# Performance work log

Measured on AMD Instinct MI355X. Metric: run time of the kernel, lower is better.

The kernel has to match this reference:

```python
import jax, jax.numpy as jnp
import numpy as np

HEAD = 16

def setup_inputs() -> dict:
    key = jax.random.key(0)
    k1, k2, k3 = jax.random.split(key, 3)
    B, S, D = 2, 2048, 1024
    x = jax.random.normal(k1, (B, S, D), dtype=jnp.float32)
    w_qkv = jax.random.normal(k2, (D, 3 * D), dtype=jnp.float32) * (1.0 / np.sqrt(D))
    b_qkv = jnp.zeros((3 * D,), dtype=jnp.float32)
    w_out = jax.random.normal(k3, (D, D), dtype=jnp.float32) * (1.0 / np.sqrt(D))
    b_out = jnp.zeros((D,), dtype=jnp.float32)
    return {"x": x, "w_qkv": w_qkv, "b_qkv": b_qkv, "w_out": w_out, "b_out": b_out}


def reference(x, w_qkv, b_qkv, w_out, b_out):
    B, S, D = x.shape
    hd = D // HEAD  # head dim
    qkv = x @ w_qkv + b_qkv                      # [B,S,3D]
    qkv = qkv.reshape(B, S, 3, HEAD, hd)
    qkv = jnp.transpose(qkv, (2, 0, 3, 1, 4))    # [3,B,H,S,hd]
    q, k, v = qkv[0], qkv[1], qkv[2]
    scores = jnp.einsum('bhqd,bhkd->bhqk', q, k)  # [B,H,S,S]
    causal = jnp.triu(jnp.ones((S, S), dtype=bool), k=1)
    scores = jnp.where(causal, -jnp.inf, scores)
    scores = scores / jnp.sqrt(jnp.asarray(hd, dtype=x.dtype))
    attn = jax.nn.softmax(scores, axis=-1)
    z = jnp.einsum('bhqk,bhkd->bhqd', attn, v)   # [B,H,S,hd]
    z = jnp.transpose(z, (0, 2, 1, 3)).reshape(B, S, D)
    out = z @ w_out + b_out
    return out
```

## Files before the change

kernel.cpp:

```cpp
#include <hip/hip_runtime.h>

#define S_LEN  2048
#define NH     16
#define HD     64
#define DMODEL 1024

using bf16x8 = __attribute__((ext_vector_type(8))) __bf16;
using f32x4  = __attribute__((ext_vector_type(4))) float;

__device__ __forceinline__ unsigned short f2bf(float f) {
    unsigned u = __float_as_uint(f);
    u += 0x7FFFu + ((u >> 16) & 1u);
    return (unsigned short)(u >> 16);
}
__device__ __forceinline__ unsigned pk_trunc(float lo, float hi) {
    return __builtin_amdgcn_perm(__float_as_uint(hi), __float_as_uint(lo), 0x07060302u);
}

#define EXP2(x) __builtin_amdgcn_exp2f(x)

#define GLDS16(gsrc, ldst) \
    __builtin_amdgcn_global_load_lds((__attribute__((address_space(1))) void*)(gsrc), \
                                     (__attribute__((address_space(3))) void*)(ldst), 16, 0, 0)

#define WAIT_LGKM0() __builtin_amdgcn_s_waitcnt(0xC07F)

#define ASM_VMCNT(n)  asm volatile("s_waitcnt vmcnt(" #n ")" ::: "memory")
#define ASM_BARRIER() asm volatile("s_barrier" ::: "memory")

__global__ __launch_bounds__(256) void prep_kernel(
    const float* __restrict__ x, const float* __restrict__ w_qkv,
    const float* __restrict__ w_out,
    unsigned short* __restrict__ xb, unsigned short* __restrict__ wqkvT,
    unsigned short* __restrict__ woutT) {
    __shared__ float T[32][33];
    int bx = blockIdx.x;
    if (bx < 4096) {
        int idx = (bx * 256 + threadIdx.x) * 4;
        float4 v = *(const float4*)(x + idx);
        ushort4 o;
        o.x = f2bf(v.x); o.y = f2bf(v.y); o.z = f2bf(v.z); o.w = f2bf(v.w);
        *(ushort4*)(xb + idx) = o;
        return;
    }
    int tb = bx - 4096;
    int tcol = tb & 127, krow = tb >> 7;
    const float* in;
    unsigned short* out;
    int N, nbx;
    if (tcol < 96) { in = w_qkv; out = wqkvT; N = 3072; nbx = tcol; }
    else           { in = w_out; out = woutT; N = 1024; nbx = tcol - 96; }
    int r  = threadIdx.x >> 3;
    int c4 = (threadIdx.x & 7) * 4;
    int kbase = krow * 32, nbase = nbx * 32;
    float4 v = *(const float4*)(in + (size_t)(kbase + r) * N + nbase + c4);
    T[r][c4 + 0] = v.x; T[r][c4 + 1] = v.y; T[r][c4 + 2] = v.z; T[r][c4 + 3] = v.w;
    __syncthreads();
    ushort4 o;
    o.x = f2bf(T[c4 + 0][r]); o.y = f2bf(T[c4 + 1][r]);
    o.z = f2bf(T[c4 + 2][r]); o.w = f2bf(T[c4 + 3][r]);
    *(ushort4*)(out + (size_t)(nbase + r) * 1024 + kbase + c4) = o;
}

template <int NI>
__device__ __forceinline__ void mfma_mainloop64(const unsigned short* __restrict__ A,
                                                const unsigned short* __restrict__ B,
                                                int K, int m0, int n0,
                                                unsigned short* As, unsigned short* Bs,
                                                f32x4 acc[4][NI]) {
    const int lane = threadIdx.x & 63, wave = threadIdx.x >> 6;
    const int quad = lane >> 4, l15 = lane & 15;
    const int wm0 = (wave >> 1) * 64, wn0 = (wave & 1) * (NI * 16);
    const int nt = K >> 6;

    auto stage = [&](int k0, int b) {
        unsigned short* Ad = As + b * 8192;
        unsigned short* Bd = Bs + b * (NI * 2048);
        #pragma unroll
        for (int j = 0; j < 4 + NI; ++j) {
            if (j < 4) {
                int c0 = j * 256 + wave * 64;
                int c  = c0 + lane;
                int r = c >> 3, pc = c & 7, q = pc ^ (r & 7);
                GLDS16(A + (size_t)(m0 + r) * K + k0 + q * 8, Ad + c0 * 8);
            } else {
                int c0 = (j - 4) * 256 + wave * 64;
                int c  = c0 + lane;
                int r = c >> 3, pc = c & 7, q = pc ^ (r & 7);
                GLDS16(B + (size_t)(n0 + r) * K + k0 + q * 8, Bd + c0 * 8);
            }
        }
    };

    auto gbody = [&](int t, int b, bool pref) {
        if (pref) {
            stage((t + 1) * 64, b ^ 1);
            if constexpr (NI == 4) { ASM_VMCNT(8); } else { ASM_VMCNT(6); }
        } else {
            ASM_VMCNT(0);
        }
        ASM_BARRIER();

        const unsigned short* Ab = As + b * 8192;
        const unsigned short* Bb = Bs + b * (NI * 2048);
        bf16x8 af[2][4], bfr[2][NI];
        #pragma unroll
        for (int mi = 0; mi < 4; ++mi) {
            int r = wm0 + mi * 16 + l15, x = r & 7;
            af[0][mi] = *(const bf16x8*)(Ab + r * 64 + ((quad    ) ^ x) * 8);
            af[1][mi] = *(const bf16x8*)(Ab + r * 64 + ((4 + quad) ^ x) * 8);
        }
        #pragma unroll
        for (int ni = 0; ni < NI; ++ni) {
            int r = wn0 + ni * 16 + l15, x = r & 7;
            bfr[0][ni] = *(const bf16x8*)(Bb + r * 64 + ((quad    ) ^ x) * 8);
            bfr[1][ni] = *(const bf16x8*)(Bb + r * 64 + ((4 + quad) ^ x) * 8);
        }
        #pragma unroll
        for (int h = 0; h < 2; ++h)
            #pragma unroll
            for (int mi = 0; mi < 4; ++mi)
                #pragma unroll
                for (int ni = 0; ni < NI; ++ni)
                    acc[mi][ni] = __builtin_amdgcn_mfma_f32_16x16x32_bf16(
                        af[h][mi], bfr[h][ni], acc[mi][ni], 0, 0, 0);
        ASM_BARRIER();
    };

    stage(0, 0);
    for (int t = 0; t < nt; t += 2) {
        gbody(t, 0, true);
        gbody(t + 1, 1, t + 2 < nt);
    }
}

__global__ __launch_bounds__(256) void gemm_qkv_kernel(
    const unsigned short* __restrict__ xb, const unsigned short* __restrict__ wT,
    const float* __restrict__ bias,
    unsigned short* __restrict__ Qt, unsigned short* __restrict__ Kh,
    unsigned short* __restrict__ Vt) {
    __shared__ __align__(16) unsigned short Sh[32768];
    unsigned short* As = Sh;
    unsigned short* Bs = Sh + 16384;

    f32x4 acc[4][4];
    #pragma unroll
    for (int i = 0; i < 4; ++i)
        #pragma unroll
        for (int j = 0; j < 4; ++j) acc[i][j] = (f32x4){0.f, 0.f, 0.f, 0.f};

    const int bid = blockIdx.x;
    const int xcd = bid & 7, slot = bid >> 3;
    const int nt = xcd * 3 + (slot % 3);
    const int mt = slot / 3;
    const int m0 = mt * 128, n0 = nt * 128;
    mfma_mainloop64<4>(xb, wT, DMODEL, m0, n0, As, Bs, acc);

    const int lane = threadIdx.x & 63, wave = threadIdx.x >> 6;
    const int quad = lane >> 4, l15 = lane & 15;
    const int wm0 = (wave >> 1) * 64, wn0 = (wave & 1) * 64;

    const int colbase = n0 + wn0;
    const int t = colbase >> 10;
    const int h = (colbase >> 6) & (NH - 1);
    const float qscale = (t == 0) ? 0.125f * 1.44269504088896f : 1.0f;
    float bv[4];
    #pragma unroll
    for (int ni = 0; ni < 4; ++ni) bv[ni] = bias[colbase + ni * 16 + l15];

    __syncthreads();
    unsigned short* Lw = Sh + wave * 1536;

    #pragma unroll
    for (int mi = 0; mi < 4; ++mi) {
        int mbase = m0 + wm0 + mi * 16;
        int b = mbase >> 11, sbase = mbase & (S_LEN - 1);
        if (t == 1) {
            #pragma unroll
            for (int ni = 0; ni < 4; ++ni)
                #pragma unroll
                for (int r = 0; r < 4; ++r)
                    Lw[(quad * 4 + r) * 72 + ni * 16 + l15] =
                        f2bf(acc[mi][ni][r] + bv[ni]);
            WAIT_LGKM0();
            int rr = lane & 15, dc = (lane >> 4) * 16;
            uint4 v0 = *(const uint4*)(Lw + rr * 72 + dc);
            uint4 v1 = *(const uint4*)(Lw + rr * 72 + dc + 8);
            unsigned short* dst =
                Kh + ((size_t)(b * NH + h) * S_LEN + sbase + rr) * HD + dc;
            *(uint4*)dst = v0;
            *(uint4*)(dst + 8) = v1;
        } else {
            #pragma unroll
            for (int ni = 0; ni < 4; ++ni)
                #pragma unroll
                for (int r = 0; r < 4; ++r)
                    Lw[(ni * 16 + l15) * 24 + quad * 4 + r] =
                        f2bf((acc[mi][ni][r] + bv[ni]) * qscale);
            WAIT_LGKM0();
            int c = lane;
            uint4 v0 = *(const uint4*)(Lw + c * 24);
            uint4 v1 = *(const uint4*)(Lw + c * 24 + 8);
            unsigned short* base = (t == 0) ? Qt : Vt;
            unsigned short* dst =
                base + ((size_t)(b * NH + h) * HD + c) * S_LEN + sbase;
            *(uint4*)dst = v0;
            *(uint4*)(dst + 8) = v1;
        }
        WAIT_LGKM0();
    }
}

__global__ __launch_bounds__(256) void gemm_out_kernel(
    const unsigned short* __restrict__ zb, const unsigned short* __restrict__ wT,
    const float* __restrict__ bias, float* __restrict__ out) {
    __shared__ __align__(16) unsigned short As[16384], Bs[8192];
    f32x4 acc[4][2];
    #pragma unroll
    for (int i = 0; i < 4; ++i)
        #pragma unroll
        for (int j = 0; j < 2; ++j) acc[i][j] = (f32x4){0.f, 0.f, 0.f, 0.f};

    const int bid = blockIdx.x;
    const int xcd = bid & 7, slot = bid >> 3;
    const int nt = xcd * 2 + (slot & 1);
    const int mt = slot >> 1;
    const int m0 = mt * 128, n0 = nt * 64;
    mfma_mainloop64<2>(zb, wT, DMODEL, m0, n0, As, Bs, acc);

    const int lane = threadIdx.x & 63, wave = threadIdx.x >> 6;
    const int quad = lane >> 4, l15 = lane & 15;
    const int wm0 = (wave >> 1) * 64, wn0 = (wave & 1) * 32;
    #pragma unroll
    for (int mi = 0; mi < 4; ++mi) {
        #pragma unroll
        for (int ni = 0; ni < 2; ++ni) {
            int col = n0 + wn0 + ni * 16 + l15;
            float bvv = bias[col];
            #pragma unroll
            for (int r = 0; r < 4; ++r)
                out[(size_t)(m0 + wm0 + mi * 16 + quad * 4 + r) * DMODEL + col] =
                    acc[mi][ni][r] + bvv;
        }
    }
}

__device__ const int g_sched[24 * 4] = {
    15,0,15,0,  15,16,31,1,  7,0,15,-1,
    14,0,14,0,  14,15,29,1,  6,0,13,-1,
    13,0,13,0,  13,14,27,1,
    12,0,12,0,  12,13,25,1,  5,0,11,-1,
    11,0,11,0,  11,12,23,1,
    10,0,10,0,  10,11,21,1,  4,0,9,-1,
     9,0,9,0,    9,10,19,1,
     8,0,8,0,    8,9,17,1,   3,0,7,-1,
     2,0,5,-1,   1,0,3,-1,   0,0,1,-1
};

__global__ __launch_bounds__(512) void attn_mfma_kernel(
    const unsigned short* __restrict__ Qt, const unsigned short* __restrict__ Kh,
    const unsigned short* __restrict__ Vt, unsigned short* __restrict__ zb,
    float* __restrict__ Zp, float* __restrict__ lp) {
    __shared__ __align__(16) unsigned short Ks[2 * 64 * 64];
    __shared__ __align__(16) unsigned short Vs[2 * 64 * 64];
    __shared__ __align__(16) unsigned short Pl[8 * 16 * 64];

    const int lane = threadIdx.x & 63, wave = threadIdx.x >> 6;
    const int quad = lane >> 4, l15 = lane & 15;
    const int bh = blockIdx.x;
    const int qt   = g_sched[blockIdx.y * 4 + 0];
    const int klo  = g_sched[blockIdx.y * 4 + 1];
    const int khi  = g_sched[blockIdx.y * 4 + 2];
    const int part = g_sched[blockIdx.y * 4 + 3];
    const int q0 = qt * 128;
    const float M0 = 12.0f;

    bf16x8 qf0, qf1;
    {
        const unsigned short* qb = Qt + (size_t)bh * HD * S_LEN + q0 + wave * 16 + l15;
        union { bf16x8 v; unsigned short u[8]; } u0, u1;
        #pragma unroll
        for (int j = 0; j < 8; ++j) {
            u0.u[j] = qb[(quad * 8 + j) * S_LEN];
            u1.u[j] = qb[(32 + quad * 8 + j) * S_LEN];
        }
        qf0 = u0.v; qf1 = u1.v;
    }

    f32x4 Z[4];
    #pragma unroll
    for (int i = 0; i < 4; ++i) Z[i] = (f32x4){0.f, 0.f, 0.f, 0.f};
    float rsum = 0.f;

    unsigned short* pw = Pl + wave * 1024;
    const int pwrow = l15 * 64;

    auto stageKV = [&](int kt, int b) {
        {
            int c0 = wave * 64;
            int c  = c0 + lane;
            int r = c >> 3, pc = c & 7, q = pc ^ (r & 7);
            GLDS16(Kh + ((size_t)bh * S_LEN + kt * 64 + r) * HD + q * 8,
                   Ks + b * 4096 + c0 * 8);
        }
        {
            int c0 = wave * 64;
            int c  = c0 + lane;
            int d = c >> 3, pc = c & 7, q = pc ^ (d & 7);
            GLDS16(Vt + ((size_t)bh * HD + d) * S_LEN + kt * 64 + q * 8,
                   Vs + b * 4096 + c0 * 8);
        }
    };

    auto body = [&](int kt, int cb, bool pref) {
        if (pref) {
            stageKV(kt + 1, cb ^ 1);
            ASM_VMCNT(2);
        } else {
            ASM_VMCNT(0);
        }
        ASM_BARRIER();

        const unsigned short* Kb = Ks + cb * 4096;
        const unsigned short* Vb = Vs + cb * 4096;

        const int kq = kt - 2 * qt;
        const int dw = (kq >= 0) ? (wave - (kq << 2)) : 7;
        if (dw >= 0) {
            const int nmax = dw < 3 ? dw : 3;
            const int qthr = dw * 16 + l15 - quad * 4;

            #pragma unroll
            for (int n = 0; n < 4; ++n) {
                int woff = pwrow + (((2 * n + (quad >> 1)) ^ (l15 & 7)) << 3) + (quad & 1) * 4;
                if (n <= nmax) {
                    int rk = n * 16 + l15;
                    int x = rk & 7;
                    bf16x8 kv0 = *(const bf16x8*)(Kb + rk * 64 + ((quad    ) ^ x) * 8);
                    bf16x8 kv1 = *(const bf16x8*)(Kb + rk * 64 + ((4 + quad) ^ x) * 8);
                    f32x4 t4 = (f32x4){-M0, -M0, -M0, -M0};
                    __builtin_amdgcn_s_setprio(1);
                    t4 = __builtin_amdgcn_mfma_f32_16x16x32_bf16(kv0, qf0, t4, 0, 0, 0);
                    t4 = __builtin_amdgcn_mfma_f32_16x16x32_bf16(kv1, qf1, t4, 0, 0, 0);
                    __builtin_amdgcn_s_setprio(0);
                    float p[4];
                    #pragma unroll
                    for (int r = 0; r < 4; ++r) {
                        p[r] = EXP2(t4[r]);
                        if ((n * 16 + r) > qthr) p[r] = 0.f;
                        rsum += p[r];
                    }
                    uint2 pk;
                    pk.x = pk_trunc(p[0], p[1]);
                    pk.y = pk_trunc(p[2], p[3]);
                    *(uint2*)(pw + woff) = pk;
                } else {
                    *(uint2*)(pw + woff) = (uint2){0u, 0u};
                }
            }

            const int khmax = (dw >> 1) < 1 ? (dw >> 1) : 1;
            for (int kh = 0; kh <= khmax; ++kh) {
                bf16x8 pa = *(const bf16x8*)(pw + pwrow + ((kh * 4 + quad) ^ (l15 & 7)) * 8);
                __builtin_amdgcn_s_setprio(1);
                #pragma unroll
                for (int ni = 0; ni < 4; ++ni) {
                    int rd = ni * 16 + l15;
                    bf16x8 vb = *(const bf16x8*)(Vb + rd * 64 + ((kh * 4 + quad) ^ (rd & 7)) * 8);
                    Z[ni] = __builtin_amdgcn_mfma_f32_16x16x32_bf16(vb, pa, Z[ni], 0, 0, 0);
                }
                __builtin_amdgcn_s_setprio(0);
            }
        }
        ASM_BARRIER();
    };

    stageKV(klo, 0);
    {
        int cnt = khi - klo + 1;
        int kt = klo;
        while (cnt >= 2) {
            body(kt, 0, true);
            body(kt + 1, 1, cnt > 2);
            kt += 2; cnt -= 2;
        }
        if (cnt == 1) body(kt, 0, false);
    }

    rsum += __shfl_xor(rsum, 16);
    rsum += __shfl_xor(rsum, 32);

    const int ql = wave * 16 + l15;
    if (part < 0) {
        const int b = bh >> 4, h = bh & (NH - 1);
        float inv = 1.f / rsum;
        size_t rowoff = (size_t)(b * S_LEN + q0 + ql) * DMODEL + h * HD;
        #pragma unroll
        for (int ni = 0; ni < 4; ++ni) {
            ushort4 o;
            o.x = f2bf(Z[ni][0] * inv);
            o.y = f2bf(Z[ni][1] * inv);
            o.z = f2bf(Z[ni][2] * inv);
            o.w = f2bf(Z[ni][3] * inv);
            *(ushort4*)(zb + rowoff + ni * 16 + quad * 4) = o;
        }
    } else {
        const int slot = (qt - 8) * 2 + part;
        float* zpo = Zp + ((size_t)(slot * 32 + bh) * 128 + ql) * 64;
        #pragma unroll
        for (int ni = 0; ni < 4; ++ni) {
            float4 st;
            st.x = Z[ni][0]; st.y = Z[ni][1]; st.z = Z[ni][2]; st.w = Z[ni][3];
            *(float4*)(zpo + ni * 16 + quad * 4) = st;
        }
        if (quad == 0)
            lp[(size_t)(slot * 32 + bh) * 128 + ql] = rsum;
    }
}

__global__ __launch_bounds__(256) void attn_merge_kernel(
    const float* __restrict__ Zp, const float* __restrict__ lp,
    unsigned short* __restrict__ zb) {
    const int bh = blockIdx.x, qi = blockIdx.y, qt = 8 + qi;
    const int t = threadIdx.x;
    const int q = t >> 1;
    const int d0 = (t & 1) << 5;
    const int s0 = qi * 2, s1 = s0 + 1;
    float l = lp[(size_t)(s0 * 32 + bh) * 128 + q] +
              lp[(size_t)(s1 * 32 + bh) * 128 + q];
    float inv = 1.f / l;
    const float* z0 = Zp + ((size_t)(s0 * 32 + bh) * 128 + q) * 64 + d0;
    const float* z1 = Zp + ((size_t)(s1 * 32 + bh) * 128 + q) * 64 + d0;
    const int b = bh >> 4, h = bh & (NH - 1);
    unsigned short* o =
        zb + (size_t)(b * S_LEN + qt * 128 + q) * DMODEL + h * HD + d0;
    #pragma unroll
    for (int i = 0; i < 32; i += 4) {
        float4 a = *(const float4*)(z0 + i);
        float4 c = *(const float4*)(z1 + i);
        ushort4 ov;
        ov.x = f2bf((a.x + c.x) * inv);
        ov.y = f2bf((a.y + c.y) * inv);
        ov.z = f2bf((a.z + c.z) * inv);
        ov.w = f2bf((a.w + c.w) * inv);
        *(ushort4*)(o + i) = ov;
    }
}

extern "C" void kernel_launch(void* const* d_in, const int* in_sizes, int n_in,
                              void* d_out, int out_size, void* d_ws, size_t ws_size,
                              hipStream_t stream)
{
    const float* x     = (const float*)d_in[0];
    const float* w_qkv = (const float*)d_in[1];
    const float* b_qkv = (const float*)d_in[2];
    const float* w_out = (const float*)d_in[3];
    const float* b_out = (const float*)d_in[4];
    float* out = (float*)d_out;

    unsigned short* wsu   = (unsigned short*)d_ws;
    unsigned short* xb    = wsu;
    unsigned short* wqkvT = xb    + (size_t)4194304;
    unsigned short* woutT = wqkvT + (size_t)3145728;
    unsigned short* Qt    = woutT + (size_t)1048576;
    unsigned short* Kh    = Qt    + (size_t)4194304;
    unsigned short* Vt    = Kh    + (size_t)4194304;
    unsigned short* zb    = Vt    + (size_t)4194304;
    float* Zp = (float*)(zb + (size_t)4194304);
    float* lp = Zp + (size_t)16 * 32 * 128 * 64;

    prep_kernel<<<dim3(8192), 256, 0, stream>>>(x, w_qkv, w_out, xb, wqkvT, woutT);

    gemm_qkv_kernel<<<dim3(768), 256, 0, stream>>>(
        xb, wqkvT, b_qkv, Qt, Kh, Vt);

    attn_mfma_kernel<<<dim3(2 * NH, 24), 512, 0, stream>>>(Qt, Kh, Vt, zb, Zp, lp);
    attn_merge_kernel<<<dim3(2 * NH, 8), 256, 0, stream>>>(Zp, lp, zb);

    gemm_out_kernel<<<dim3(512), 256, 0, stream>>>(
        zb, woutT, b_out, out);
}
```

Baseline: 181.5 us.

## Load GEMM B operand directly from global into registers, bypassing LDS

```diff
diff --git a/kernel.cpp b/kernel.cpp
--- a/kernel.cpp
+++ b/kernel.cpp
@@ -63,75 +63,74 @@
 }
 
 template <int NI>
-__device__ __forceinline__ void mfma_mainloop64(const unsigned short* __restrict__ A,
-                                                const unsigned short* __restrict__ B,
-                                                int K, int m0, int n0,
-                                                unsigned short* As, unsigned short* Bs,
-                                                f32x4 acc[4][NI]) {
+__device__ __forceinline__ void mfma_mainloop_bd(
+    const unsigned short* __restrict__ A, const unsigned short* __restrict__ B,
+    int K, int m0, int n0, unsigned short* As, f32x4 acc[4][NI]) {
     const int lane = threadIdx.x & 63, wave = threadIdx.x >> 6;
     const int quad = lane >> 4, l15 = lane & 15;
     const int wm0 = (wave >> 1) * 64, wn0 = (wave & 1) * (NI * 16);
     const int nt = K >> 6;
-
-    auto stage = [&](int k0, int b) {
-        unsigned short* Ad = As + b * 8192;
-        unsigned short* Bd = Bs + b * (NI * 2048);
-        #pragma unroll
-        for (int j = 0; j < 4 + NI; ++j) {
-            if (j < 4) {
-                int c0 = j * 256 + wave * 64;
-                int c  = c0 + lane;
-                int r = c >> 3, pc = c & 7, q = pc ^ (r & 7);
-                GLDS16(A + (size_t)(m0 + r) * K + k0 + q * 8, Ad + c0 * 8);
-            } else {
-                int c0 = (j - 4) * 256 + wave * 64;
-                int c  = c0 + lane;
-                int r = c >> 3, pc = c & 7, q = pc ^ (r & 7);
-                GLDS16(B + (size_t)(n0 + r) * K + k0 + q * 8, Bd + c0 * 8);
-            }
-        }
-    };
-
-    auto gbody = [&](int t, int b, bool pref) {
-        if (pref) {
-            stage((t + 1) * 64, b ^ 1);
-            if constexpr (NI == 4) { ASM_VMCNT(8); } else { ASM_VMCNT(6); }
+    const unsigned short* Bw = B + (size_t)(n0 + wn0 + l15) * K + quad * 8;
+
+#define STAGE_A(k0, b) { \
+    unsigned short* Ad = As + (b) * 8192; \
+    _Pragma("unroll") \
+    for (int j = 0; j < 4; ++j) { \
+        int c0 = j * 256 + wave * 64; \
+        int c  = c0 + lane; \
+        int r = c >> 3, pc = c & 7, q = pc ^ (r & 7); \
+        GLDS16(A + (size_t)(m0 + r) * K + (k0) + q * 8, Ad + c0 * 8); \
+    } }
+
+#define LOAD_B(k0, br) { \
+    _Pragma("unroll") \
+    for (int ni = 0; ni < NI; ++ni) { \
+        br[0][ni] = *(const bf16x8*)(Bw + (size_t)(ni * 16) * K + (k0)); \
+        br[1][ni] = *(const bf16x8*)(Bw + (size_t)(ni * 16) * K + (k0) + 32); \
+    } }
+
+#define COMPUTE(b, br) { \
+    const unsigned short* Ab = As + (b) * 8192; \
+    bf16x8 af[2][4]; \
+    _Pragma("unroll") \
+    for (int mi = 0; mi < 4; ++mi) { \
+        int r = wm0 + mi * 16 + l15, x = r & 7; \
+        af[0][mi] = *(const bf16x8*)(Ab + r * 64 + ((quad    ) ^ x) * 8); \
+        af[1][mi] = *(const bf16x8*)(Ab + r * 64 + ((4 + quad) ^ x) * 8); \
+    } \
+    _Pragma("unroll") \
+    for (int h = 0; h < 2; ++h) \
+        _Pragma("unroll") \
+        for (int mi = 0; mi < 4; ++mi) \
+            _Pragma("unroll") \
+            for (int ni = 0; ni < NI; ++ni) \
+                acc[mi][ni] = __builtin_amdgcn_mfma_f32_16x16x32_bf16( \
+                    af[h][mi], br[h][ni], acc[mi][ni], 0, 0, 0); }
+
+    bf16x8 brX[2][NI], brY[2][NI];
+    STAGE_A(0, 0);
+    LOAD_B(0, brX);
+    for (int t = 0; t < nt; t += 2) {
+        STAGE_A((t + 1) * 64, 1);
+        LOAD_B((t + 1) * 64, brY);
+        if constexpr (NI == 4) { ASM_VMCNT(12); } else { ASM_VMCNT(8); }
+        ASM_BARRIER();
+        COMPUTE(0, brX);
+        ASM_BARRIER();
+        if (t + 2 < nt) {
+            STAGE_A((t + 2) * 64, 0);
+            LOAD_B((t + 2) * 64, brX);
+            if constexpr (NI == 4) { ASM_VMCNT(12); } else { ASM_VMCNT(8); }
         } else {
             ASM_VMCNT(0);
         }
         ASM_BARRIER();
-
-        const unsigned short* Ab = As + b * 8192;
-        const unsigned short* Bb = Bs + b * (NI * 2048);
-        bf16x8 af[2][4], bfr[2][NI];
-        #pragma unroll
-        for (int mi = 0; mi < 4; ++mi) {
-            int r = wm0 + mi * 16 + l15, x = r & 7;
-            af[0][mi] = *(const bf16x8*)(Ab + r * 64 + ((quad    ) ^ x) * 8);
-            af[1][mi] = *(const bf16x8*)(Ab + r * 64 + ((4 + quad) ^ x) * 8);
-        }
-        #pragma unroll
-        for (int ni = 0; ni < NI; ++ni) {
-            int r = wn0 + ni * 16 + l15, x = r & 7;
-            bfr[0][ni] = *(const bf16x8*)(Bb + r * 64 + ((quad    ) ^ x) * 8);
-            bfr[1][ni] = *(const bf16x8*)(Bb + r * 64 + ((4 + quad) ^ x) * 8);
-        }
-        #pragma unroll
-        for (int h = 0; h < 2; ++h)
-            #pragma unroll
-            for (int mi = 0; mi < 4; ++mi)
-                #pragma unroll
-                for (int ni = 0; ni < NI; ++ni)
-                    acc[mi][ni] = __builtin_amdgcn_mfma_f32_16x16x32_bf16(
-                        af[h][mi], bfr[h][ni], acc[mi][ni], 0, 0, 0);
-        ASM_BARRIER();
-    };
-
-    stage(0, 0);
-    for (int t = 0; t < nt; t += 2) {
-        gbody(t, 0, true);
-        gbody(t + 1, 1, t + 2 < nt);
-    }
+        COMPUTE(1, brY);
+        ASM_BARRIER();
+    }
+#undef STAGE_A
+#undef LOAD_B
+#undef COMPUTE
 }
 
 __global__ __launch_bounds__(256) void gemm_qkv_kernel(
@@ -139,9 +138,8 @@
     const float* __restrict__ bias,
     unsigned short* __restrict__ Qt, unsigned short* __restrict__ Kh,
     unsigned short* __restrict__ Vt) {
-    __shared__ __align__(16) unsigned short Sh[32768];
+    __shared__ __align__(16) unsigned short Sh[16384];
     unsigned short* As = Sh;
-    unsigned short* Bs = Sh + 16384;
 
     f32x4 acc[4][4];
     #pragma unroll
@@ -154,7 +152,7 @@
     const int nt = xcd * 3 + (slot % 3);
     const int mt = slot / 3;
     const int m0 = mt * 128, n0 = nt * 128;
-    mfma_mainloop64<4>(xb, wT, DMODEL, m0, n0, As, Bs, acc);
+    mfma_mainloop_bd<4>(xb, wT, DMODEL, m0, n0, As, acc);
 
     const int lane = threadIdx.x & 63, wave = threadIdx.x >> 6;
     const int quad = lane >> 4, l15 = lane & 15;
@@ -214,7 +212,7 @@
 __global__ __launch_bounds__(256) void gemm_out_kernel(
     const unsigned short* __restrict__ zb, const unsigned short* __restrict__ wT,
     const float* __restrict__ bias, float* __restrict__ out) {
-    __shared__ __align__(16) unsigned short As[16384], Bs[8192];
+    __shared__ __align__(16) unsigned short As[16384];
     f32x4 acc[4][2];
     #pragma unroll
     for (int i = 0; i < 4; ++i)
@@ -226,7 +224,7 @@
     const int nt = xcd * 2 + (slot & 1);
     const int mt = slot >> 1;
     const int m0 = mt * 128, n0 = nt * 64;
-    mfma_mainloop64<2>(zb, wT, DMODEL, m0, n0, As, Bs, acc);
+    mfma_mainloop_bd<2>(zb, wT, DMODEL, m0, n0, As, acc);
 
     const int lane = threadIdx.x & 63, wave = threadIdx.x >> 6;
     const int quad = lane >> 4, l15 = lane & 15;
```

Measured after the change: 224.0 us. 1.23x slower.

## Triple-buffer A tiles and use one barrier per k-step in GEMM mainloop

Applied to the files above, without the earlier changes.

```diff
diff --git a/kernel.cpp b/kernel.cpp
--- a/kernel.cpp
+++ b/kernel.cpp
@@ -62,47 +62,53 @@
     *(ushort4*)(out + (size_t)(nbase + r) * 1024 + kbase + c4) = o;
 }
 
-template <int NI>
+template <int NI, int NT>
 __device__ __forceinline__ void mfma_mainloop64(const unsigned short* __restrict__ A,
                                                 const unsigned short* __restrict__ B,
-                                                int K, int m0, int n0,
+                                                int m0, int n0,
                                                 unsigned short* As, unsigned short* Bs,
                                                 f32x4 acc[4][NI]) {
+    constexpr int K = NT * 64;
     const int lane = threadIdx.x & 63, wave = threadIdx.x >> 6;
     const int quad = lane >> 4, l15 = lane & 15;
     const int wm0 = (wave >> 1) * 64, wn0 = (wave & 1) * (NI * 16);
-    const int nt = K >> 6;
-
-    auto stage = [&](int k0, int b) {
-        unsigned short* Ad = As + b * 8192;
-        unsigned short* Bd = Bs + b * (NI * 2048);
-        #pragma unroll
-        for (int j = 0; j < 4 + NI; ++j) {
-            if (j < 4) {
-                int c0 = j * 256 + wave * 64;
-                int c  = c0 + lane;
-                int r = c >> 3, pc = c & 7, q = pc ^ (r & 7);
-                GLDS16(A + (size_t)(m0 + r) * K + k0 + q * 8, Ad + c0 * 8);
-            } else {
-                int c0 = (j - 4) * 256 + wave * 64;
-                int c  = c0 + lane;
-                int r = c >> 3, pc = c & 7, q = pc ^ (r & 7);
-                GLDS16(B + (size_t)(n0 + r) * K + k0 + q * 8, Bd + c0 * 8);
-            }
+
+    auto stageA = [&](int t) {
+        unsigned short* Ad = As + (t % 3) * 8192;
+        #pragma unroll
+        for (int j = 0; j < 4; ++j) {
+            int c0 = j * 256 + wave * 64;
+            int c  = c0 + lane;
+            int r = c >> 3, pc = c & 7, q = pc ^ (r & 7);
+            GLDS16(A + (size_t)(m0 + r) * K + t * 64 + q * 8, Ad + c0 * 8);
         }
     };
-
-    auto gbody = [&](int t, int b, bool pref) {
-        if (pref) {
-            stage((t + 1) * 64, b ^ 1);
-            if constexpr (NI == 4) { ASM_VMCNT(8); } else { ASM_VMCNT(6); }
-        } else {
-            ASM_VMCNT(0);
-        }
+    auto stageB = [&](int t) {
+        unsigned short* Bd = Bs + (t & 1) * (NI * 2048);
+        #pragma unroll
+        for (int j = 0; j < NI; ++j) {
+            int c0 = j * 256 + wave * 64;
+            int c  = c0 + lane;
+            int r = c >> 3, pc = c & 7, q = pc ^ (r & 7);
+            GLDS16(B + (size_t)(n0 + r) * K + t * 64 + q * 8, Bd + c0 * 8);
+        }
+    };
+
+    stageB(0); stageA(0);
+    stageB(1); stageA(1);
+    stageA(2);
+
+    #pragma unroll
+    for (int t = 0; t < NT; ++t) {
+        if (t < NT - 1) { ASM_VMCNT(4); } else { ASM_VMCNT(0); }
         ASM_BARRIER();
-
-        const unsigned short* Ab = As + b * 8192;
-        const unsigned short* Bb = Bs + b * (NI * 2048);
+        if (t >= 1) {
+            if (t + 1 < NT) stageB(t + 1);
+            if (t + 2 < NT) stageA(t + 2);
+        }
+
+        const unsigned short* Ab = As + (t % 3) * 8192;
+        const unsigned short* Bb = Bs + (t & 1) * (NI * 2048);
         bf16x8 af[2][4], bfr[2][NI];
         #pragma unroll
         for (int mi = 0; mi < 4; ++mi) {
@@ -124,13 +130,6 @@
                 for (int ni = 0; ni < NI; ++ni)
                     acc[mi][ni] = __builtin_amdgcn_mfma_f32_16x16x32_bf16(
                         af[h][mi], bfr[h][ni], acc[mi][ni], 0, 0, 0);
-        ASM_BARRIER();
-    };
-
-    stage(0, 0);
-    for (int t = 0; t < nt; t += 2) {
-        gbody(t, 0, true);
-        gbody(t + 1, 1, t + 2 < nt);
     }
 }
 
@@ -139,9 +138,9 @@
     const float* __restrict__ bias,
     unsigned short* __restrict__ Qt, unsigned short* __restrict__ Kh,
     unsigned short* __restrict__ Vt) {
-    __shared__ __align__(16) unsigned short Sh[32768];
+    __shared__ __align__(16) unsigned short Sh[40960];
     unsigned short* As = Sh;
-    unsigned short* Bs = Sh + 16384;
+    unsigned short* Bs = Sh + 24576;
 
     f32x4 acc[4][4];
     #pragma unroll
@@ -154,7 +153,7 @@
     const int nt = xcd * 3 + (slot % 3);
     const int mt = slot / 3;
     const int m0 = mt * 128, n0 = nt * 128;
-    mfma_mainloop64<4>(xb, wT, DMODEL, m0, n0, As, Bs, acc);
+    mfma_mainloop64<4, 16>(xb, wT, m0, n0, As, Bs, acc);
 
     const int lane = threadIdx.x & 63, wave = threadIdx.x >> 6;
     const int quad = lane >> 4, l15 = lane & 15;
@@ -214,7 +213,7 @@
 __global__ __launch_bounds__(256) void gemm_out_kernel(
     const unsigned short* __restrict__ zb, const unsigned short* __restrict__ wT,
     const float* __restrict__ bias, float* __restrict__ out) {
-    __shared__ __align__(16) unsigned short As[16384], Bs[8192];
+    __shared__ __align__(16) unsigned short As[24576], Bs[8192];
     f32x4 acc[4][2];
     #pragma unroll
     for (int i = 0; i < 4; ++i)
@@ -226,7 +225,7 @@
     const int nt = xcd * 2 + (slot & 1);
     const int mt = slot >> 1;
     const int m0 = mt * 128, n0 = nt * 64;
-    mfma_mainloop64<2>(zb, wT, DMODEL, m0, n0, As, Bs, acc);
+    mfma_mainloop64<2, 16>(zb, wT, m0, n0, As, Bs, acc);
 
     const int lane = threadIdx.x & 63, wave = threadIdx.x >> 6;
     const int quad = lane >> 4, l15 = lane & 15;
```

New measurement: 169.0 us. 6.9% less time.
